# Performance work log

Hardware: AMD Instinct MI355X
Metric: run time of the kernel (lower is better)

## Reference

```python
import jax, jax.numpy as jnp
import numpy as np

N = 16384; E = 262144; B = 8
IN = 768; HID = 256; H1 = 4; OUT = 128; H2 = 2

def setup_inputs() -> dict:
    key = jax.random.key(0)
    ks = jax.random.split(key, 16)
    s = 0.02
    def p(k, shape):
        return jax.random.normal(k, shape, jnp.float32) * s
    return {
        "x": jax.random.normal(ks[0], (N, IN), jnp.float32),
        "edge_index": jax.random.randint(ks[1], (2, E), 0, N),
        "batch": jnp.sort(jax.random.randint(ks[2], (N,), 0, B)),
        "W1": p(ks[3], (H1 * HID, IN)),
        "a_src1": p(ks[4], (H1, HID)),
        "a_dst1": p(ks[5], (H1, HID)),
        "b1": jnp.zeros((H1 * HID,), jnp.float32),
        "W2": p(ks[6], (H2 * OUT, H1 * HID)),
        "a_src2": p(ks[7], (H2, OUT)),
        "a_dst2": p(ks[8], (H2, OUT)),
        "b2": jnp.zeros((OUT,), jnp.float32),
        "proj_W": p(ks[9], (768, OUT)),
        "proj_b": jnp.zeros((768,), jnp.float32),
        "ln_g": jnp.ones((768,), jnp.float32),
        "ln_b": jnp.zeros((768,), jnp.float32),
        "rh_W1": p(ks[10], (32, OUT + 2)),
        "rh_b1": jnp.zeros((32,), jnp.float32),
        "rh_W2": p(ks[11], (1, 32)),
        "rh_b2": jnp.zeros((1,), jnp.float32),
        "num_graphs": B,
    }

def _gat(x, src, dst, W, a_s, a_d, bias, heads, ch, concat, n):
    # PyG GATConv (shared src/dst lin): h = x W^T -> [n, heads, ch]
    h = (x @ W.T).reshape(n, heads, ch)
    al_s = (h * a_s).sum(-1)  # [n, heads]
    al_d = (h * a_d).sum(-1)
    e = jax.nn.leaky_relu(al_s[src] + al_d[dst], 0.2)  # [E', heads]
    # segment softmax over incoming edges of each destination node
    m = jax.lax.stop_gradient(jax.ops.segment_max(e, dst, num_segments=n))
    ex = jnp.exp(e - m[dst])
    den = jax.ops.segment_sum(ex, dst, num_segments=n)
    w = ex / (den[dst] + 1e-16)
    out = jax.ops.segment_sum(w[:, :, None] * h[src], dst, num_segments=n)
    if concat:
        return out.reshape(n, heads * ch) + bias
    return out.mean(1) + bias

def reference(x, edge_index, batch, W1, a_src1, a_dst1, b1, W2, a_src2, a_dst2, b2,
              proj_W, proj_b, ln_g, ln_b, rh_W1, rh_b1, rh_W2, rh_b2, num_graphs):
    n = x.shape[0]
    src0, dst0 = edge_index[0], edge_index[1]
    loop = jnp.arange(n)  # GATConv adds self-loops by default
    src = jnp.concatenate([src0, loop])
    dst = jnp.concatenate([dst0, loop])
    h1 = jax.nn.elu(_gat(x, src, dst, W1, a_src1, a_dst1, b1, H1, HID, True, n))
    h2 = jax.nn.elu(_gat(h1, src, dst, W2, a_src2, a_dst2, b2, H2, OUT, False, n))
    # global mean pool per graph
    n_g = jax.ops.segment_sum(jnp.ones((n,), x.dtype), batch, num_segments=num_graphs)
    pooled = jax.ops.segment_sum(h2, batch, num_segments=num_graphs) / jnp.maximum(n_g, 1.0)[:, None]
    pe = pooled @ proj_W.T + proj_b
    mu = pe.mean(-1, keepdims=True)
    var = pe.var(-1, keepdims=True)
    struct_embed = (pe - mu) / jnp.sqrt(var + 1e-5) * ln_g + ln_b
    # topology stats from ORIGINAL edges (no self-loops), per original code
    e_g = jax.ops.segment_sum(jnp.ones((src0.shape[0],), x.dtype), batch[src0], num_segments=num_graphs)
    stats = jnp.stack([e_g / (n_g + 1e-6), jnp.log(n_g + 1.0)], axis=-1)  # [B, 2]
    ri = jnp.concatenate([pooled, stats], axis=-1)
    hid = jax.nn.relu(ri @ rh_W1.T + rh_b1)
    prop_risk = jax.nn.sigmoid(hid @ rh_W2.T + rh_b2)[:, 0]
    return struct_embed, h2, prop_risk
```

## Files before the change

kernel.cpp:

```cpp
#include <hip/hip_runtime.h>
#include <math.h>

#define NN    16384
#define EE    262144
#define ET    (EE + NN)
#define NB    8
#define IN_F  768
#define HID1  256
#define H1    4
#define D1    (H1*HID1)
#define OUT2  128
#define H2    2
#define D2    (H2*OUT2)

typedef __attribute__((ext_vector_type(8))) _Float16 f16x8;
typedef __attribute__((ext_vector_type(4))) float f32x4;

__device__ __forceinline__ float hf2f(unsigned short u) {
    union { unsigned short u; _Float16 h; } c; c.u = u; return (float)c.h;
}
__device__ __forceinline__ unsigned short f2hf(float f) {
    union { unsigned short u; _Float16 h; } c; c.h = (_Float16)f; return c.u;
}


__device__ __forceinline__ void grid_barrier(int* cnt, int* gen, int nb) {
    __syncthreads();
    if (threadIdx.x == 0) {
        int g = __hip_atomic_load(gen, __ATOMIC_RELAXED, __HIP_MEMORY_SCOPE_AGENT);
        int v = __hip_atomic_fetch_add(cnt, 1, __ATOMIC_ACQ_REL, __HIP_MEMORY_SCOPE_AGENT);
        if (v == nb - 1) {
            __hip_atomic_store(cnt, 0, __ATOMIC_RELAXED, __HIP_MEMORY_SCOPE_AGENT);
            __hip_atomic_fetch_add(gen, 1, __ATOMIC_RELEASE, __HIP_MEMORY_SCOPE_AGENT);
        } else {
            while (__hip_atomic_load(gen, __ATOMIC_ACQUIRE, __HIP_MEMORY_SCOPE_AGENT) == g)
                __builtin_amdgcn_s_sleep(2);
        }
    }
    __syncthreads();
}


__global__ void prep_kernel(const float* __restrict__ x,  unsigned short* __restrict__ xo,
                            const float* __restrict__ w1, unsigned short* __restrict__ w1o,
                            const float* __restrict__ w2, unsigned short* __restrict__ w2o,
                            float4* __restrict__ zbase, int zunits) {
    const int n1 = NN * IN_F / 4;
    const int n2 = D1 * IN_F / 4;
    const int n3 = D2 * D1 / 4;
    int i = blockIdx.x * blockDim.x + threadIdx.x;
    if (i < n1 + n2 + n3) {
        const float* src; unsigned short* dst; int j;
        if (i < n1)           { src = x;  dst = xo;  j = i; }
        else if (i < n1 + n2) { src = w1; dst = w1o; j = i - n1; }
        else                  { src = w2; dst = w2o; j = i - n1 - n2; }
        float4 v = ((const float4*)src)[j];
        ushort4 h;
        h.x = f2hf(v.x); h.y = f2hf(v.y); h.z = f2hf(v.z); h.w = f2hf(v.w);
        ((ushort4*)dst)[j] = h;
    } else {
        int j = i - (n1 + n2 + n3);
        if (j < zunits) zbase[j] = make_float4(0.f, 0.f, 0.f, 0.f);
    }
}


__global__ void hist_kernel(const int* __restrict__ ei, const int* __restrict__ batch,
                            int* __restrict__ deg, int* __restrict__ n_g, int* __restrict__ e_cnt) {
    __shared__ int le[NB], ln[NB];
    int tid = threadIdx.x;
    if (tid < NB) { le[tid] = 0; ln[tid] = 0; }
    __syncthreads();
    int t = blockIdx.x * blockDim.x + tid;
    if (t < EE) {
        int s = ei[t];
        int d = ei[EE + t];
        atomicAdd(&deg[d], 1);
        atomicAdd(&le[batch[s]], 1);
    }
    if (t < NN) {
        atomicAdd(&ln[batch[t]], 1);
    }
    __syncthreads();
    if (tid < NB) {
        if (le[tid]) atomicAdd(&e_cnt[tid], le[tid]);
        if (ln[tid]) atomicAdd(&n_g[tid], ln[tid]);
    }
}

__global__ __launch_bounds__(1024) void scan_kernel(const int* __restrict__ deg, int* __restrict__ row_ptr) {
    __shared__ int sums[1024];
    int t = threadIdx.x;
    int base = t * 16;
    int local[16];
    int acc = 0;
#pragma unroll
    for (int i = 0; i < 16; i++) { local[i] = acc; acc += deg[base + i] + 1; }
    sums[t] = acc;
    __syncthreads();
    for (int off = 1; off < 1024; off <<= 1) {
        int v = (t >= off) ? sums[t - off] : 0;
        __syncthreads();
        sums[t] += v;
        __syncthreads();
    }
    int prev = (t == 0) ? 0 : sums[t - 1];
#pragma unroll
    for (int i = 0; i < 16; i++) row_ptr[base + i] = prev + local[i];
    if (t == 1023) row_ptr[NN] = sums[1023];
}


__device__ __forceinline__ void ld_lds16(const unsigned short* g, unsigned short* l) {
    __builtin_amdgcn_global_load_lds((__attribute__((address_space(1))) void*)g,
                                     (__attribute__((address_space(3))) void*)l, 16, 0, 0);
}

#define BM 128
#define BN 128
#define BK 32

__global__ __launch_bounds__(256) void gemm_mfma(const unsigned short* __restrict__ A,
                                                 const unsigned short* __restrict__ B,
                                                 unsigned short* __restrict__ C,
                                                 int M, int N, int K,
                                                 int gemmBlocks,
                                                 const int* __restrict__ ei,
                                                 const int* __restrict__ row_ptr,
                                                 int* __restrict__ cursor,
                                                 int* __restrict__ colidx) {
    if ((int)blockIdx.x >= gemmBlocks) {
        int t = (blockIdx.x - gemmBlocks) * 256 + threadIdx.x;
        if (t < ET) {
            int s, d;
            if (t < EE) { s = ei[t]; d = ei[EE + t]; }
            else        { s = d = t - EE; }
            int pos = row_ptr[d] + atomicAdd(&cursor[d], 1);
            colidx[pos] = s;
        }
        return;
    }

    __shared__ __align__(16) unsigned short sA[BM * BK];
    __shared__ __align__(16) unsigned short sB[BN * BK];
    int t = threadIdx.x;
    int lane = t & 63, wave = t >> 6;

    int NC = N / BN;
    int b = blockIdx.x;
    int xcd = b & 7;
    int idx = b >> 3;
    int c = idx % NC;
    int rg = idx / NC;
    int bm = (rg * 8 + xcd) * BM;
    int bn = c * BN;

    int wm = (wave & 1) * 64, wn = (wave >> 1) * 64;

    const unsigned short* gbase;
    unsigned short* lbase;
    {
        int hrow = (wave & 1) * 64;
        if (wave < 2) { gbase = A + (size_t)(bm + hrow) * K; lbase = sA + hrow * BK; }
        else          { gbase = B + (size_t)(bn + hrow) * K; lbase = sB + hrow * BK; }
    }
    int schunk = (lane & 3) ^ ((lane >> 3) & 3);
    const unsigned short* gsrc = gbase + (size_t)(lane >> 2) * K + schunk * 8;

    f32x4 zero = {0.f, 0.f, 0.f, 0.f};
    f32x4 acc[4][4];
#pragma unroll
    for (int i = 0; i < 4; i++)
#pragma unroll
        for (int j = 0; j < 4; j++) acc[i][j] = zero;

    int row16 = lane & 15;
    int kq = ((lane >> 4) ^ ((row16 >> 1) & 3)) * 8;

    for (int k0 = 0; k0 < K; k0 += BK) {
#pragma unroll
        for (int i = 0; i < 4; i++)
            ld_lds16(gsrc + k0 + (size_t)(i * 16) * K, lbase + i * 16 * BK);
        __syncthreads();

        f16x8 ah[4], bh[4];
#pragma unroll
        for (int mt = 0; mt < 4; mt++)
            ah[mt] = *(const f16x8*)&sA[(wm + mt * 16 + row16) * BK + kq];
#pragma unroll
        for (int nt = 0; nt < 4; nt++)
            bh[nt] = *(const f16x8*)&sB[(wn + nt * 16 + row16) * BK + kq];
#pragma unroll
        for (int mt = 0; mt < 4; mt++)
#pragma unroll
            for (int nt = 0; nt < 4; nt++)
                acc[mt][nt] = __builtin_amdgcn_mfma_f32_16x16x32_f16(ah[mt], bh[nt], acc[mt][nt], 0, 0, 0);
        __syncthreads();
    }

    int crow0 = bm + wm + (lane >> 4) * 4;
    int ccol0 = bn + wn + row16;
#pragma unroll
    for (int mt = 0; mt < 4; mt++)
#pragma unroll
        for (int nt = 0; nt < 4; nt++)
#pragma unroll
            for (int reg = 0; reg < 4; reg++)
                C[(size_t)(crow0 + mt * 16 + reg) * N + ccol0 + nt * 16] = f2hf(acc[mt][nt][reg]);
}


__global__ __launch_bounds__(256) void al1_kernel(const unsigned short* __restrict__ h,
                                                  const float* __restrict__ a_s,
                                                  const float* __restrict__ a_d,
                                                  float* __restrict__ als,
                                                  float* __restrict__ ald) {
    int node = blockIdx.x;
    int head = threadIdx.x >> 6;
    int lane = threadIdx.x & 63;
    int co = head * HID1 + lane * 4;
    ushort4 hv = *(const ushort4*)(h + (size_t)node * D1 + co);
    float4 as = *(const float4*)(a_s + co);
    float4 ad = *(const float4*)(a_d + co);
    float h0 = hf2f(hv.x), h1 = hf2f(hv.y), h2 = hf2f(hv.z), h3 = hf2f(hv.w);
    float ss = h0 * as.x + h1 * as.y + h2 * as.z + h3 * as.w;
    float sd = h0 * ad.x + h1 * ad.y + h2 * ad.z + h3 * ad.w;
#pragma unroll
    for (int off = 32; off; off >>= 1) {
        ss += __shfl_down(ss, off);
        sd += __shfl_down(sd, off);
    }
    if (lane == 0) {
        als[node * H1 + head] = ss;
        ald[node * H1 + head] = sd;
    }
}

__global__ __launch_bounds__(256) void al2_kernel(const unsigned short* __restrict__ h,
                                                  const float* __restrict__ a_s,
                                                  const float* __restrict__ a_d,
                                                  float* __restrict__ als,
                                                  float* __restrict__ ald) {
    int unit = threadIdx.x >> 6;
    int node = blockIdx.x * 2 + (unit >> 1);
    int head = unit & 1;
    int lane = threadIdx.x & 63;
    int co = head * OUT2 + lane * 2;
    ushort2 hv = *(const ushort2*)(h + (size_t)node * D2 + co);
    float2 as = *(const float2*)(a_s + co);
    float2 ad = *(const float2*)(a_d + co);
    float h0 = hf2f(hv.x), h1 = hf2f(hv.y);
    float ss = h0 * as.x + h1 * as.y;
    float sd = h0 * ad.x + h1 * ad.y;
#pragma unroll
    for (int off = 32; off; off >>= 1) {
        ss += __shfl_down(ss, off);
        sd += __shfl_down(sd, off);
    }
    if (lane == 0) {
        als[node * H2 + head] = ss;
        ald[node * H2 + head] = sd;
    }
}

__device__ __forceinline__ float leaky(float v) { return v > 0.f ? v : 0.2f * v; }
__device__ __forceinline__ float elu1(float v) { return v > 0.f ? v : (__expf(v) - 1.f); }


__global__ __launch_bounds__(256) void agg1_kernel(const unsigned short* __restrict__ h,
                                                   const float* __restrict__ als,
                                                   const float* __restrict__ ald,
                                                   const int* __restrict__ row_ptr,
                                                   const int* __restrict__ colidx,
                                                   const float* __restrict__ bias,
                                                   unsigned short* __restrict__ outp) {
    int b = blockIdx.x;
    int s = b & 7;
    int g = b >> 3;
    int wave = threadIdx.x >> 6;
    int lane = threadIdx.x & 63;
    int lanesel = lane & 32;
    int l5 = lane & 31;
    int d = g * 8 + wave * 2 + (lanesel >> 5);
    int head = s >> 1;
    int start = row_ptr[d], end = row_ptr[d + 1];
    int deg = end - start;
    int degO = __shfl_xor(deg, 32);
    int degmax = max(deg, degO);
    float ald_h = ald[d * H1 + head];
    unsigned choff = (unsigned)(s * 128 + l5 * 4);

    float a0 = 0.f, a1 = 0.f, a2 = 0.f, a3 = 0.f;
    float wsum = 0.f;

    for (int c0 = 0; c0 < degmax; c0 += 32) {
        int ee = start + c0 + l5;
        int idx = ee < end ? ee : end - 1;
        int sL = colidx[idx];
        float ev = leaky(als[(sL << 2) + head] + ald_h);
        float wL = (ee < end) ? __expf(ev) : 0.f;
        float ws = wL;
        ws += __shfl_xor(ws, 16); ws += __shfl_xor(ws, 8);
        ws += __shfl_xor(ws, 4);  ws += __shfl_xor(ws, 2);  ws += __shfl_xor(ws, 1);
        wsum += ws;

        int n = degmax - c0; if (n > 32) n = 32;
        int n8 = (n + 7) & ~7;
        for (int k = 0; k < n8; k += 8) {
            ushort4 hv[8]; float wv[8];
#pragma unroll
            for (int j = 0; j < 8; j++) {
                int src = k + j + lanesel;
                int ssj = __shfl(sL, src);
                wv[j]   = __shfl(wL, src);
                hv[j] = *(const ushort4*)(h + (((unsigned)ssj << 10) + choff));
            }
#pragma unroll
            for (int j = 0; j < 8; j++) {
                float w = wv[j];
                a0 += w * hf2f(hv[j].x); a1 += w * hf2f(hv[j].y);
                a2 += w * hf2f(hv[j].z); a3 += w * hf2f(hv[j].w);
            }
        }
    }

    float sinv = 1.f / (wsum + 1e-16f);
    float4 bv = *(const float4*)(bias + s * 128 + l5 * 4);
    float o0 = elu1(a0 * sinv + bv.x);
    float o1 = elu1(a1 * sinv + bv.y);
    float o2 = elu1(a2 * sinv + bv.z);
    float o3 = elu1(a3 * sinv + bv.w);
    unsigned long long pk = (unsigned long long)f2hf(o0)
                          | ((unsigned long long)f2hf(o1) << 16)
                          | ((unsigned long long)f2hf(o2) << 32)
                          | ((unsigned long long)f2hf(o3) << 48);
    size_t o = (size_t)d * D1 + choff;
    __builtin_nontemporal_store(pk, (unsigned long long*)(outp + o));
}


__global__ __launch_bounds__(256) void agg2_kernel(const unsigned short* __restrict__ h,
                                                   const float* __restrict__ als,
                                                   const float* __restrict__ ald,
                                                   const int* __restrict__ row_ptr,
                                                   const int* __restrict__ colidx,
                                                   const float* __restrict__ bias,
                                                   float* __restrict__ out) {
    int wave = threadIdx.x >> 6;
    int lane = threadIdx.x & 63;
    int lanesel = lane & 32;
    int l5 = lane & 31;
    int head = lanesel >> 5;
    int d = blockIdx.x * 4 + wave;
    int start = row_ptr[d], end = row_ptr[d + 1];
    int deg = end - start;
    float ald_h = ald[d * H2 + head];
    unsigned ch4 = (unsigned)(lane << 2);

    float a0 = 0.f, a1 = 0.f, a2 = 0.f, a3 = 0.f;
    float wsum = 0.f;

    for (int c0 = 0; c0 < deg; c0 += 32) {
        int ee = start + c0 + l5;
        int idx = ee < end ? ee : end - 1;
        int sL = colidx[idx];
        float ev = leaky(als[(sL << 1) + head] + ald_h);
        float wL = (ee < end) ? __expf(ev) : 0.f;
        float ws = wL;
        ws += __shfl_xor(ws, 16); ws += __shfl_xor(ws, 8);
        ws += __shfl_xor(ws, 4);  ws += __shfl_xor(ws, 2);  ws += __shfl_xor(ws, 1);
        wsum += ws;

        int n = deg - c0; if (n > 32) n = 32;
        int n8 = (n + 7) & ~7;
        for (int k = 0; k < n8; k += 8) {
            ushort4 hv[8]; float wv[8];
#pragma unroll
            for (int j = 0; j < 8; j++) {
                int ssj = __builtin_amdgcn_readlane(sL, k + j);
                wv[j] = __shfl(wL, k + j + lanesel);
                hv[j] = *(const ushort4*)(h + (((unsigned)ssj << 8) + ch4));
            }
#pragma unroll
            for (int j = 0; j < 8; j++) {
                float w = wv[j];
                a0 += w * hf2f(hv[j].x); a1 += w * hf2f(hv[j].y);
                a2 += w * hf2f(hv[j].z); a3 += w * hf2f(hv[j].w);
            }
        }
    }

    float sinv = 1.f / (wsum + 1e-16f);
    float r0 = a0 * sinv, r1 = a1 * sinv, r2 = a2 * sinv, r3 = a3 * sinv;
    r0 += __shfl_xor(r0, 32);
    r1 += __shfl_xor(r1, 32);
    r2 += __shfl_xor(r2, 32);
    r3 += __shfl_xor(r3, 32);
    if (lane < 32) {
        float4 bv = *(const float4*)(bias + (l5 << 2));
        float4 o;
        o.x = elu1(r0 * 0.5f + bv.x);
        o.y = elu1(r1 * 0.5f + bv.y);
        o.z = elu1(r2 * 0.5f + bv.z);
        o.w = elu1(r3 * 0.5f + bv.w);
        *(float4*)(out + (size_t)d * OUT2 + (l5 << 2)) = o;
    }
}


__global__ __launch_bounds__(256) void poolfinal_kernel(const float* __restrict__ h2,
                                                        const int* __restrict__ batch,
                                                        float* __restrict__ pooled_sum,
                                                        const int* __restrict__ n_g_i,
                                                        const int* __restrict__ e_cnt,
                                                        const float* __restrict__ projW,
                                                        const float* __restrict__ projb,
                                                        const float* __restrict__ lng,
                                                        const float* __restrict__ lnb,
                                                        const float* __restrict__ rhW1,
                                                        const float* __restrict__ rhb1,
                                                        const float* __restrict__ rhW2,
                                                        const float* __restrict__ rhb2,
                                                        float* __restrict__ out_se,
                                                        float* __restrict__ out_risk,
                                                        int* bc, int* bg) {
    int t = threadIdx.x;
    __shared__ float pooled[OUT2];
    __shared__ float pe[768];
    __shared__ float red[256];
    __shared__ float hid[32];
    __shared__ float stat_mu, stat_inv;

    {
        int c = t & 127;
        int half = t >> 7;
        int n0 = blockIdx.x * 256 + half;
        int nend = blockIdx.x * 256 + 256;
        float acc = 0.f;
        int curg = batch[n0];
        for (int n = n0; n < nend; n += 2) {
            int g = batch[n];
            if (g != curg) {
                atomicAdd(&pooled_sum[curg * OUT2 + c], acc);
                acc = 0.f; curg = g;
            }
            acc += h2[(size_t)n * OUT2 + c];
        }
        atomicAdd(&pooled_sum[curg * OUT2 + c], acc);
    }
    grid_barrier(bc, bg, 64);
    if (blockIdx.x >= NB) return;

    int gb = blockIdx.x;
    float ng = (float)n_g_i[gb];
    if (t < OUT2) {
        float ps = __hip_atomic_load(&pooled_sum[gb * OUT2 + t], __ATOMIC_RELAXED,
                                     __HIP_MEMORY_SCOPE_AGENT);
        pooled[t] = ps / fmaxf(ng, 1.0f);
    }
    __syncthreads();

    for (int j = t; j < 768; j += 256) {
        const float* wr = projW + (size_t)j * OUT2;
        float s = projb[j];
        for (int c = 0; c < OUT2; c++) s += pooled[c] * wr[c];
        pe[j] = s;
    }
    __syncthreads();

    float ls = 0.f, lq = 0.f;
    for (int j = t; j < 768; j += 256) { float v = pe[j]; ls += v; lq += v * v; }
    red[t] = ls;
    __syncthreads();
    for (int off = 128; off; off >>= 1) { if (t < off) red[t] += red[t + off]; __syncthreads(); }
    float tot = red[0];
    __syncthreads();
    red[t] = lq;
    __syncthreads();
    for (int off = 128; off; off >>= 1) { if (t < off) red[t] += red[t + off]; __syncthreads(); }
    float totq = red[0];
    if (t == 0) {
        float mu = tot / 768.f;
        float var = totq / 768.f - mu * mu;
        stat_mu = mu;
        stat_inv = 1.f / sqrtf(var + 1e-5f);
    }
    __syncthreads();
    float mu = stat_mu, inv = stat_inv;
    for (int j = t; j < 768; j += 256)
        out_se[(size_t)gb * 768 + j] = (pe[j] - mu) * inv * lng[j] + lnb[j];

    float s0 = (float)e_cnt[gb] / (ng + 1e-6f);
    float s1 = logf(ng + 1.0f);
    if (t < 32) {
        const float* wr = rhW1 + t * (OUT2 + 2);
        float s = rhb1[t];
        for (int c = 0; c < OUT2; c++) s += pooled[c] * wr[c];
        s += s0 * wr[OUT2] + s1 * wr[OUT2 + 1];
        hid[t] = fmaxf(s, 0.f);
    }
    __syncthreads();
    if (t == 0) {
        float s = rhb2[0];
        for (int k = 0; k < 32; k++) s += hid[k] * rhW2[k];
        out_risk[gb] = 1.f / (1.f + __expf(-s));
    }
}


extern "C" void kernel_launch(void* const* d_in, const int* in_sizes, int n_in,
                              void* d_out, int out_size, void* d_ws, size_t ws_size,
                              hipStream_t stream) {
    const float* x     = (const float*)d_in[0];
    const int*   ei    = (const int*)  d_in[1];
    const int*   batch = (const int*)  d_in[2];
    const float* W1    = (const float*)d_in[3];
    const float* a_s1  = (const float*)d_in[4];
    const float* a_d1  = (const float*)d_in[5];
    const float* b1    = (const float*)d_in[6];
    const float* W2    = (const float*)d_in[7];
    const float* a_s2  = (const float*)d_in[8];
    const float* a_d2  = (const float*)d_in[9];
    const float* b2    = (const float*)d_in[10];
    const float* projW = (const float*)d_in[11];
    const float* projb = (const float*)d_in[12];
    const float* lng   = (const float*)d_in[13];
    const float* lnb   = (const float*)d_in[14];
    const float* rhW1  = (const float*)d_in[15];
    const float* rhb1  = (const float*)d_in[16];
    const float* rhW2  = (const float*)d_in[17];
    const float* rhb2  = (const float*)d_in[18];

    char* ws = (char*)d_ws;
    size_t off = 0;
    auto alloc = [&](size_t bytes) -> void* {
        void* p = ws + off;
        off += (bytes + 255) & ~(size_t)255;
        return p;
    };

    unsigned short* regionA = (unsigned short*)alloc((size_t)NN * D1 * 2);
    unsigned short* x_f  = regionA;
    unsigned short* h1a  = regionA;

    unsigned short* h1f  = (unsigned short*)alloc((size_t)NN * D1 * 2);
    unsigned short* h2ft = (unsigned short*)alloc((size_t)NN * D2 * 2);
    unsigned short* W1f  = (unsigned short*)alloc((size_t)D1 * IN_F * 2);
    unsigned short* W2f  = (unsigned short*)alloc((size_t)D2 * D1 * 2);
    float* als1   = (float*)alloc((size_t)NN * H1 * 4);
    float* ald1   = (float*)alloc((size_t)NN * H1 * 4);
    float* als2   = (float*)alloc((size_t)NN * H2 * 4);
    float* ald2   = (float*)alloc((size_t)NN * H2 * 4);
    int*   row_ptr= (int*)  alloc((size_t)(NN + 1) * 4);
    int*   colidx = (int*)  alloc((size_t)ET * 4);
    size_t zoff = off;
    int*   deg    = (int*)  alloc((size_t)NN * 4);
    int*   cursor = (int*)  alloc((size_t)NN * 4);
    int*   n_g    = (int*)  alloc((size_t)NB * 4);
    int*   e_cnt  = (int*)  alloc((size_t)NB * 4);
    float* pooled = (float*)alloc((size_t)NB * OUT2 * 4);
    int*   bars   = (int*)  alloc((size_t)8 * 4);
    size_t zbytes = off - zoff;

    float* out_se   = (float*)d_out;
    float* h2out    = out_se + NB * 768;
    float* out_risk = h2out + (size_t)NN * OUT2;

    {
        int ntot = NN * IN_F / 4 + D1 * IN_F / 4 + D2 * D1 / 4;
        int zunits = (int)(zbytes / 16);
        int grid = (ntot + zunits + 255) / 256;
        prep_kernel<<<grid, 256, 0, stream>>>(x, x_f, W1, W1f, W2, W2f,
                                              (float4*)(ws + zoff), zunits);
    }

    hist_kernel<<<(EE + 255) / 256, 256, 0, stream>>>(ei, batch, deg, n_g, e_cnt);
    scan_kernel<<<1, 1024, 0, stream>>>(deg, row_ptr);

    {
        int gb = (NN / BM) * (D1 / BN);
        int sb = (ET + 255) / 256;
        gemm_mfma<<<gb + sb, 256, 0, stream>>>(x_f, W1f, h1f, NN, D1, IN_F,
                                               gb, ei, row_ptr, cursor, colidx);
    }

    al1_kernel<<<NN, 256, 0, stream>>>(h1f, a_s1, a_d1, als1, ald1);
    agg1_kernel<<<NN, 256, 0, stream>>>(h1f, als1, ald1, row_ptr, colidx, b1, h1a);

    {
        int gb = (NN / BM) * (D2 / BN);
        gemm_mfma<<<gb, 256, 0, stream>>>(h1a, W2f, h2ft, NN, D2, D1,
                                          gb, ei, row_ptr, cursor, colidx);
    }
    al2_kernel<<<NN / 2, 256, 0, stream>>>(h2ft, a_s2, a_d2, als2, ald2);
    agg2_kernel<<<NN / 4, 256, 0, stream>>>(h2ft, als2, ald2, row_ptr, colidx, b2, h2out);

    poolfinal_kernel<<<NN / 256, 256, 0, stream>>>(h2out, batch, pooled, n_g, e_cnt,
                                                   projW, projb, lng, lnb,
                                                   rhW1, rhb1, rhW2, rhb2,
                                                   out_se, out_risk, &bars[0], &bars[1]);
}
```

Measured before the change: 398.3 us.

## Spread mean-pool over more blocks with float4 loads and block-level reduction

The pooling phase of the final kernel now launches 256 blocks of 64 nodes instead of 64 blocks of 256 nodes. Each thread accumulates float4 slices over 8 nodes. When a block's nodes all belong to one graph, partial sums are reduced through shuffles and shared memory, so only 32 threads issue atomics. This aims to raise memory-level parallelism and cut atomic traffic in the pooling stage, in exchange for a grid barrier across more blocks.

Result: faster. 375.9 us (-5.6%).

```diff
diff --git a/kernel.cpp b/kernel.cpp
--- a/kernel.cpp
+++ b/kernel.cpp
@@ -425,6 +425,7 @@
                                                         float* __restrict__ out_risk,
                                                         int* bc, int* bg) {
     int t = threadIdx.x;
+    __shared__ float4 pr[4][32];
     __shared__ float pooled[OUT2];
     __shared__ float pe[768];
     __shared__ float red[256];
@@ -432,23 +433,53 @@
     __shared__ float stat_mu, stat_inv;
 
     {
-        int c = t & 127;
-        int half = t >> 7;
-        int n0 = blockIdx.x * 256 + half;
-        int nend = blockIdx.x * 256 + 256;
-        float acc = 0.f;
-        int curg = batch[n0];
-        for (int n = n0; n < nend; n += 2) {
-            int g = batch[n];
-            if (g != curg) {
-                atomicAdd(&pooled_sum[curg * OUT2 + c], acc);
-                acc = 0.f; curg = g;
+        int col = (t & 31) << 2;
+        int chain = t >> 5;
+        int nbase = blockIdx.x * 64;
+        int n0 = nbase + chain * 8;
+        float ax = 0.f, ay = 0.f, az = 0.f, aw = 0.f;
+        int gfirst = batch[nbase];
+        if (gfirst == batch[nbase + 63]) {
+#pragma unroll
+            for (int i = 0; i < 8; i++) {
+                float4 v = *(const float4*)(h2 + (size_t)(n0 + i) * OUT2 + col);
+                ax += v.x; ay += v.y; az += v.z; aw += v.w;
             }
-            acc += h2[(size_t)n * OUT2 + c];
+            ax += __shfl_xor(ax, 32); ay += __shfl_xor(ay, 32);
+            az += __shfl_xor(az, 32); aw += __shfl_xor(aw, 32);
+            int wv = t >> 6, l5 = t & 31;
+            if ((t & 32) == 0) pr[wv][l5] = make_float4(ax, ay, az, aw);
+            __syncthreads();
+            if (t < 32) {
+                float4 s0 = pr[0][t], s1 = pr[1][t], s2 = pr[2][t], s3 = pr[3][t];
+                float sx = (s0.x + s1.x) + (s2.x + s3.x);
+                float sy = (s0.y + s1.y) + (s2.y + s3.y);
+                float sz = (s0.z + s1.z) + (s2.z + s3.z);
+                float sw = (s0.w + s1.w) + (s2.w + s3.w);
+                float* dst = pooled_sum + gfirst * OUT2 + (t << 2);
+                atomicAdd(dst + 0, sx); atomicAdd(dst + 1, sy);
+                atomicAdd(dst + 2, sz); atomicAdd(dst + 3, sw);
+            }
+        } else {
+            int curg = batch[n0];
+#pragma unroll
+            for (int i = 0; i < 8; i++) {
+                int g = batch[n0 + i];
+                if (g != curg) {
+                    float* dst = pooled_sum + curg * OUT2 + col;
+                    atomicAdd(dst + 0, ax); atomicAdd(dst + 1, ay);
+                    atomicAdd(dst + 2, az); atomicAdd(dst + 3, aw);
+                    ax = ay = az = aw = 0.f; curg = g;
+                }
+                float4 v = *(const float4*)(h2 + (size_t)(n0 + i) * OUT2 + col);
+                ax += v.x; ay += v.y; az += v.z; aw += v.w;
+            }
+            float* dst = pooled_sum + curg * OUT2 + col;
+            atomicAdd(dst + 0, ax); atomicAdd(dst + 1, ay);
+            atomicAdd(dst + 2, az); atomicAdd(dst + 3, aw);
         }
-        atomicAdd(&pooled_sum[curg * OUT2 + c], acc);
-    }
-    grid_barrier(bc, bg, 64);
+    }
+    grid_barrier(bc, bg, 256);
     if (blockIdx.x >= NB) return;
 
     int gb = blockIdx.x;
@@ -595,8 +626,8 @@
     al2_kernel<<<NN / 2, 256, 0, stream>>>(h2ft, a_s2, a_d2, als2, ald2);
     agg2_kernel<<<NN / 4, 256, 0, stream>>>(h2ft, als2, ald2, row_ptr, colidx, b2, h2out);
 
-    poolfinal_kernel<<<NN / 256, 256, 0, stream>>>(h2out, batch, pooled, n_g, e_cnt,
-                                                   projW, projb, lng, lnb,
-                                                   rhW1, rhb1, rhW2, rhb2,
-                                                   out_se, out_risk, &bars[0], &bars[1]);
-}
+    poolfinal_kernel<<<NN / 64, 256, 0, stream>>>(h2out, batch, pooled, n_g, e_cnt,
+                                                  projW, projb, lng, lnb,
+                                                  rhW1, rhb1, rhW2, rhb2,
+                                                  out_se, out_risk, &bars[0], &bars[1]);
+}
```
